# Performance work log

Hardware: AMD Instinct MI355X
Metric: run time of the kernel (lower is better)

The kernel has to match this reference:

```python
import jax, jax.numpy as jnp
import numpy as np

N0, N1, N2 = 20000, 15000, 15000
N = N0 + N1 + N2            # total nodes
E = 800000                  # edges (avg degree 16)
H, C = 128, 64


def setup_inputs() -> dict:
    key = jax.random.key(0)
    ks = jax.random.split(key, 16)
    s = 0.05  # weight scale
    return {
        "feat0": jax.random.normal(ks[0], (N0, 512), jnp.float32),
        "feat1": jax.random.normal(ks[1], (N1, 256), jnp.float32),
        "feat2": jax.random.normal(ks[2], (N2, 128), jnp.float32),
        "W0": jax.random.normal(ks[3], (512, H), jnp.float32) * s,
        "b0": jnp.zeros((H,), jnp.float32),
        "W1": jax.random.normal(ks[4], (256, H), jnp.float32) * s,
        "b1": jnp.zeros((H,), jnp.float32),
        "W2": jax.random.normal(ks[5], (128, H), jnp.float32) * s,
        "b2": jnp.zeros((H,), jnp.float32),
        "bias_l0": jnp.zeros((H,), jnp.float32),
        "W_l1": jax.random.normal(ks[6], (H, H), jnp.float32) * s,
        "b_l1": jnp.zeros((H,), jnp.float32),
        "W_l2": jax.random.normal(ks[7], (H, C), jnp.float32) * s,
        "b_l2": jnp.zeros((C,), jnp.float32),
        "src": jax.random.randint(ks[8], (E,), 0, N, jnp.int32),
        "dst": jax.random.randint(ks[9], (E,), 0, N, jnp.int32),
    }


def _norms(src, dst):
    # DGL GraphConv norm='both': src side uses out-degree, dst side in-degree
    ones = jnp.ones((E,), jnp.float32)
    deg_out = jax.ops.segment_sum(ones, src, num_segments=N)
    deg_in = jax.ops.segment_sum(ones, dst, num_segments=N)
    return jnp.maximum(deg_out, 1.0) ** -0.5, jnp.maximum(deg_in, 1.0) ** -0.5


def _agg(h, src, dst, norm_src, norm_dst):
    # normalized sparse aggregation: D_in^{-1/2} A D_out^{-1/2} h
    m = (h * norm_src[:, None])[src]                     # [E, d] gather
    a = jax.ops.segment_sum(m, dst, num_segments=N)      # [N, d] scatter-add
    return a * norm_dst[:, None]


def reference(feat0, feat1, feat2, W0, b0, W1, b1, W2, b2,
              bias_l0, W_l1, b_l1, W_l2, b_l2, src, dst):
    # per-node-type linear projections, concatenated along node axis
    h = jnp.concatenate([feat0 @ W0 + b0,
                         feat1 @ W1 + b1,
                         feat2 @ W2 + b2], axis=0)       # [N, H]
    ns, nd = _norms(src, dst)
    # layer 0: GraphConv(weight=False) -> agg + bias + relu (dropout = eval identity)
    h = jax.nn.relu(_agg(h, src, dst, ns, nd) + bias_l0)
    # layer 1: agg + linear + relu
    h = jax.nn.relu(_agg(h, src, dst, ns, nd) @ W_l1 + b_l1)
    # layer 2: agg + linear (no activation)
    h = _agg(h, src, dst, ns, nd) @ W_l2 + b_l2          # [N, C]
    return h
```

## Files before the change

kernel.cpp:

```cpp
#include <hip/hip_runtime.h>
#include <hip/hip_fp16.h>

#define N_NODES 50000
#define N0_ 20000
#define N1_ 15000
#define N2_ 15000
#define E_EDGES 800000
#define H_ 128
#define C_ 64

#define PB0 ((N0_ + 63) / 64)
#define PB1 ((N1_ + 63) / 64)
#define PB2 ((N2_ + 63) / 64)
#define PB_TOTAL (PB0 + PB1 + PB2)
#define EB ((E_EDGES + 255) / 256)
#define SB ((N_NODES + 255) / 256)

typedef _Float16 half4_t __attribute__((ext_vector_type(4)));
typedef _Float16 half8_t __attribute__((ext_vector_type(8)));
typedef float f32x4 __attribute__((ext_vector_type(4)));

__device__ __forceinline__ float4 load_a4(const float* A, size_t idx) {
    return *reinterpret_cast<const float4*>(&A[idx]);
}
__device__ __forceinline__ float4 load_a4(const __half* A, size_t idx) {
    __half2 p0 = *reinterpret_cast<const __half2*>(&A[idx]);
    __half2 p1 = *reinterpret_cast<const __half2*>(&A[idx + 2]);
    float2 f0 = __half22float2(p0), f1 = __half22float2(p1);
    return make_float4(f0.x, f0.y, f1.x, f1.y);
}


template <int TN, bool BIAS, bool RELU, bool SCALE, typename IT, typename OT>
__device__ __forceinline__ void gemm_block(
    const IT* __restrict__ A, const float* __restrict__ W,
    const float* __restrict__ bias, const float* __restrict__ rowscale,
    OT* __restrict__ out, int M, int K, int m0, float* As, float* Bs) {
    constexpr int NJ = TN / 32;
    constexpr int TN4 = TN / 4;
    int tid = threadIdx.x;
    int tx = tid & 31;
    int ty = tid >> 5;

    float acc[8][NJ];
#pragma unroll
    for (int i = 0; i < 8; i++)
#pragma unroll
        for (int j = 0; j < NJ; j++) acc[i][j] = 0.f;

    for (int k0 = 0; k0 < K; k0 += 32) {
#pragma unroll
        for (int t0 = 0; t0 < 2; t0++) {
            int t = tid + t0 * 256;
            int row = t >> 3;
            int c = t & 7;
            float4 v = make_float4(0.f, 0.f, 0.f, 0.f);
            if (m0 + row < M) v = load_a4(A, (size_t)(m0 + row) * K + k0 + c * 4);
            As[(c * 4 + 0) * 68 + row] = v.x;
            As[(c * 4 + 1) * 68 + row] = v.y;
            As[(c * 4 + 2) * 68 + row] = v.z;
            As[(c * 4 + 3) * 68 + row] = v.w;
        }
#pragma unroll
        for (int t0 = 0; t0 < 32 * TN4 / 256; t0++) {
            int t = tid + t0 * 256;
            int r = t / TN4;
            int c4 = t % TN4;
            *reinterpret_cast<float4*>(&Bs[r * TN + c4 * 4]) =
                *reinterpret_cast<const float4*>(&W[(size_t)(k0 + r) * TN + c4 * 4]);
        }
        __syncthreads();
#pragma unroll 8
        for (int k = 0; k < 32; k++) {
            float4 a0 = *reinterpret_cast<float4*>(&As[k * 68 + ty * 8]);
            float4 a1 = *reinterpret_cast<float4*>(&As[k * 68 + ty * 8 + 4]);
            float ar[8] = {a0.x, a0.y, a0.z, a0.w, a1.x, a1.y, a1.z, a1.w};
            float br[NJ];
#pragma unroll
            for (int j = 0; j < NJ; j++) br[j] = Bs[k * TN + tx + 32 * j];
#pragma unroll
            for (int i = 0; i < 8; i++)
#pragma unroll
                for (int j = 0; j < NJ; j++) acc[i][j] = fmaf(ar[i], br[j], acc[i][j]);
        }
        __syncthreads();
    }
#pragma unroll
    for (int i = 0; i < 8; i++) {
        int row = m0 + ty * 8 + i;
        if (row < M) {
            float sc = SCALE ? rowscale[row] : 1.f;
#pragma unroll
            for (int j = 0; j < NJ; j++) {
                float v = acc[i][j] + (BIAS ? bias[tx + 32 * j] : 0.f);
                if (RELU) v = fmaxf(v, 0.f);
                v *= sc;
                out[(size_t)row * TN + tx + 32 * j] = (OT)v;
            }
        }
    }
}


__global__ __launch_bounds__(256) void k1_proj_rank(
    const float* __restrict__ feat0, const float* __restrict__ feat1, const float* __restrict__ feat2,
    const float* __restrict__ W0, const float* __restrict__ b0,
    const float* __restrict__ W1, const float* __restrict__ b1,
    const float* __restrict__ W2, const float* __restrict__ b2,
    __half* __restrict__ h0h,
    const int* __restrict__ src, const int* __restrict__ dst,
    int* __restrict__ cnt, int* __restrict__ degO, int* __restrict__ rank) {
    __shared__ _Float16 smem[15360];
    int bid = blockIdx.x;
    int tid = threadIdx.x;
    if (bid < PB_TOTAL) {
        const float* A; const float* Wp; const float* bp; int M, K, m0;
        if (bid < PB0) {
            A = feat0; Wp = W0; bp = b0; M = N0_; K = 512; m0 = bid * 64;
        } else if (bid < PB0 + PB1) {
            A = feat1; Wp = W1; bp = b1; M = N1_; K = 256; m0 = (bid - PB0) * 64;
        } else {
            A = feat2; Wp = W2; bp = b2; M = N2_; K = 128; m0 = (bid - PB0 - PB1) * 64;
        }
        size_t obase = (bid < PB0) ? 0 : ((bid < PB0 + PB1) ? (size_t)N0_ * H_
                                                            : (size_t)(N0_ + N1_) * H_);
        _Float16* Ah = smem;
        _Float16* Al = smem + 2560;
        _Float16* Bh = smem + 5120;
        _Float16* Bl = smem + 10240;

        int wv = tid >> 6;
        int lane = tid & 63;
        int lm = lane & 15;
        int ks = lane >> 4;

        f32x4 acc[8];
#pragma unroll
        for (int j = 0; j < 8; j++)
#pragma unroll
            for (int r = 0; r < 4; r++) acc[j][r] = 0.f;

        for (int k0 = 0; k0 < K; k0 += 32) {
#pragma unroll
            for (int t0 = 0; t0 < 2; t0++) {
                int idx = tid + t0 * 256;
                int row = idx >> 3;
                int c = idx & 7;
                float4 v = make_float4(0.f, 0.f, 0.f, 0.f);
                if (m0 + row < M)
                    v = *reinterpret_cast<const float4*>(&A[(size_t)(m0 + row) * K + k0 + c * 4]);
                _Float16 hx = (_Float16)v.x, hy = (_Float16)v.y;
                _Float16 hz = (_Float16)v.z, hw = (_Float16)v.w;
                half4_t hi = {hx, hy, hz, hw};
                half4_t lo = {(_Float16)(v.x - (float)hx), (_Float16)(v.y - (float)hy),
                              (_Float16)(v.z - (float)hz), (_Float16)(v.w - (float)hw)};
                *reinterpret_cast<half4_t*>(&Ah[row * 40 + c * 4]) = hi;
                *reinterpret_cast<half4_t*>(&Al[row * 40 + c * 4]) = lo;
            }
#pragma unroll
            for (int t0 = 0; t0 < 4; t0++) {
                int idx = tid + t0 * 256;
                int kr = idx >> 5;
                int c4 = idx & 31;
                float4 v = *reinterpret_cast<const float4*>(&Wp[(size_t)(k0 + kr) * 128 + c4 * 4]);
                float f[4] = {v.x, v.y, v.z, v.w};
#pragma unroll
                for (int j = 0; j < 4; j++) {
                    _Float16 hi = (_Float16)f[j];
                    Bh[(c4 * 4 + j) * 40 + kr] = hi;
                    Bl[(c4 * 4 + j) * 40 + kr] = (_Float16)(f[j] - (float)hi);
                }
            }
            __syncthreads();
            half8_t ah = *reinterpret_cast<half8_t*>(&Ah[(16 * wv + lm) * 40 + ks * 8]);
            half8_t al = *reinterpret_cast<half8_t*>(&Al[(16 * wv + lm) * 40 + ks * 8]);
#pragma unroll
            for (int j = 0; j < 8; j++) {
                half8_t bh = *reinterpret_cast<half8_t*>(&Bh[(16 * j + lm) * 40 + ks * 8]);
                half8_t bl = *reinterpret_cast<half8_t*>(&Bl[(16 * j + lm) * 40 + ks * 8]);
                acc[j] = __builtin_amdgcn_mfma_f32_16x16x32_f16(ah, bh, acc[j], 0, 0, 0);
                acc[j] = __builtin_amdgcn_mfma_f32_16x16x32_f16(al, bh, acc[j], 0, 0, 0);
                acc[j] = __builtin_amdgcn_mfma_f32_16x16x32_f16(ah, bl, acc[j], 0, 0, 0);
            }
            __syncthreads();
        }
#pragma unroll
        for (int j = 0; j < 8; j++) {
            int colg = 16 * j + lm;
            float bb = bp[colg];
#pragma unroll
            for (int r = 0; r < 4; r++) {
                int row = m0 + 16 * wv + ks * 4 + r;
                if (row < M) h0h[obase + (size_t)row * H_ + colg] = (__half)(acc[j][r] + bb);
            }
        }
    } else {
        int e = (bid - PB_TOTAL) * 256 + tid;
        if (e < E_EDGES) {
            rank[e] = atomicAdd(&cnt[dst[e]], 1);
            atomicAdd(&degO[src[e]], 1);
        }
    }
}


__global__ __launch_bounds__(256) void scan1_kernel(
    const int* __restrict__ cnt, int* __restrict__ pre, int* __restrict__ blocksum) {
    __shared__ int buf[256];
    int t = threadIdx.x;
    int i = blockIdx.x * 256 + t;
    int tot = (i < N_NODES) ? cnt[i] : 0;
    buf[t] = tot;
    __syncthreads();
#pragma unroll
    for (int off = 1; off < 256; off <<= 1) {
        int v = (t >= off) ? buf[t - off] : 0;
        __syncthreads();
        buf[t] += v;
        __syncthreads();
    }
    if (i < N_NODES) pre[i] = buf[t] - tot;
    if (t == 255) blocksum[blockIdx.x] = buf[255];
}

__global__ __launch_bounds__(256) void scan2_kernel(
    const int* __restrict__ blocksum, int* __restrict__ blockoff, int* __restrict__ rowptr) {
    __shared__ int buf[256];
    int t = threadIdx.x;
    int v = (t < SB) ? blocksum[t] : 0;
    buf[t] = v;
    __syncthreads();
#pragma unroll
    for (int off = 1; off < 256; off <<= 1) {
        int u = (t >= off) ? buf[t - off] : 0;
        __syncthreads();
        buf[t] += u;
        __syncthreads();
    }
    if (t < SB) blockoff[t] = buf[t] - v;
    if (t == 255) rowptr[N_NODES] = buf[255];
}

__global__ __launch_bounds__(256) void scan3_fill_kernel(
    const int* __restrict__ cnt, const int* __restrict__ degO, const int* __restrict__ pre,
    const int* __restrict__ blockoff, int* __restrict__ rowptr,
    float* __restrict__ ns, float* __restrict__ nd,
    const int* __restrict__ src, const int* __restrict__ dst,
    const int* __restrict__ rank, int* __restrict__ col) {
    int bid = blockIdx.x;
    if (bid < SB) {
        int i = bid * 256 + threadIdx.x;
        if (i < N_NODES) {
            rowptr[i] = blockoff[bid] + pre[i];
            ns[i] = rsqrtf(fmaxf((float)degO[i], 1.0f));
            nd[i] = rsqrtf(fmaxf((float)cnt[i], 1.0f));
        }
    } else {
        int e = (bid - SB) * 256 + threadIdx.x;
        if (e < E_EDGES) {
            int d = dst[e];
            int rp = blockoff[d >> 8] + pre[d];
            col[rp + rank[e]] = src[e];
        }
    }
}


template <int CH, int NSLOAD, int EPI, int OUTH>
__global__ __launch_bounds__(256) void agg_h_kernel(
    const __half* __restrict__ h, const int* __restrict__ rowptr,
    const int* __restrict__ col, const float* __restrict__ ns,
    const float* __restrict__ nd, const float* __restrict__ bias,
    void* __restrict__ out) {
    constexpr int L = CH / 8;
    constexpr int EPW = 64 / L;
    int node = blockIdx.x * 4 + (threadIdx.x >> 6);
    if (node >= N_NODES) return;
    int lane = threadIdx.x & 63;
    int li = lane & (L - 1);
    int g = lane / L;
    const uint4* __restrict__ h8 = (const uint4*)h;
    int beg = rowptr[node], end = rowptr[node + 1];
    float a0[8] = {0.f, 0.f, 0.f, 0.f, 0.f, 0.f, 0.f, 0.f};
    float a1[8] = {0.f, 0.f, 0.f, 0.f, 0.f, 0.f, 0.f, 0.f};
    union U8 { uint4 u; __half2 h2[4]; };
    int e = beg + g;
    for (; e + EPW < end; e += 2 * EPW) {
        int s0 = col[e], s1 = col[e + EPW];
        U8 u0, u1;
        u0.u = h8[(size_t)s0 * L + li];
        u1.u = h8[(size_t)s1 * L + li];
        float w0 = NSLOAD ? ns[s0] : 1.f;
        float w1 = NSLOAD ? ns[s1] : 1.f;
#pragma unroll
        for (int p = 0; p < 4; p++) {
            float2 f0 = __half22float2(u0.h2[p]);
            float2 f1 = __half22float2(u1.h2[p]);
            if (NSLOAD) {
                a0[2 * p] = fmaf(w0, f0.x, a0[2 * p]);
                a0[2 * p + 1] = fmaf(w0, f0.y, a0[2 * p + 1]);
                a1[2 * p] = fmaf(w1, f1.x, a1[2 * p]);
                a1[2 * p + 1] = fmaf(w1, f1.y, a1[2 * p + 1]);
            } else {
                a0[2 * p] += f0.x;
                a0[2 * p + 1] += f0.y;
                a1[2 * p] += f1.x;
                a1[2 * p + 1] += f1.y;
            }
        }
    }
    if (e < end) {
        int s = col[e];
        U8 u0;
        u0.u = h8[(size_t)s * L + li];
        float w0 = NSLOAD ? ns[s] : 1.f;
#pragma unroll
        for (int p = 0; p < 4; p++) {
            float2 f0 = __half22float2(u0.h2[p]);
            if (NSLOAD) {
                a0[2 * p] = fmaf(w0, f0.x, a0[2 * p]);
                a0[2 * p + 1] = fmaf(w0, f0.y, a0[2 * p + 1]);
            } else {
                a0[2 * p] += f0.x;
                a0[2 * p + 1] += f0.y;
            }
        }
    }
#pragma unroll
    for (int j = 0; j < 8; j++) {
        float v = a0[j] + a1[j];
#pragma unroll
        for (int off = 32; off >= L; off >>= 1) v += __shfl_xor(v, off);
        a0[j] = v;
    }
    if (lane < L) {
        float w = nd[node];
#pragma unroll
        for (int j = 0; j < 8; j++) a0[j] *= w;
        if (EPI == 1) {
            float sc = ns[node];
#pragma unroll
            for (int j = 0; j < 8; j++)
                a0[j] = fmaxf(a0[j] + bias[li * 8 + j], 0.f) * sc;
        } else if (EPI == 2) {
#pragma unroll
            for (int j = 0; j < 8; j++) a0[j] += bias[li * 8 + j];
        }
        if (OUTH) {
            union { uint4 u; __half hh[8]; } cv;
#pragma unroll
            for (int j = 0; j < 8; j++) cv.hh[j] = __float2half(a0[j]);
            ((uint4*)out)[(size_t)node * L + li] = cv.u;
        } else {
            float4* o4 = (float4*)out;
            o4[(size_t)node * (CH / 4) + li * 2] = make_float4(a0[0], a0[1], a0[2], a0[3]);
            o4[(size_t)node * (CH / 4) + li * 2 + 1] = make_float4(a0[4], a0[5], a0[6], a0[7]);
        }
    }
}


template <int TN, bool BIAS, bool RELU, bool SCALE, typename IT, typename OT>
__global__ __launch_bounds__(256) void gemm_kernel(
    const IT* __restrict__ A, const float* __restrict__ W,
    const float* __restrict__ bias, const float* __restrict__ rowscale,
    OT* __restrict__ out, int M, int K) {
    __shared__ float As[32 * 68];
    __shared__ float Bs[32 * TN];
    gemm_block<TN, BIAS, RELU, SCALE, IT, OT>(A, W, bias, rowscale, out, M, K, blockIdx.x * 64, As, Bs);
}


extern "C" void kernel_launch(void* const* d_in, const int* in_sizes, int n_in,
                              void* d_out, int out_size, void* d_ws, size_t ws_size,
                              hipStream_t stream) {
    const float* feat0 = (const float*)d_in[0];
    const float* feat1 = (const float*)d_in[1];
    const float* feat2 = (const float*)d_in[2];
    const float* W0 = (const float*)d_in[3];
    const float* b0 = (const float*)d_in[4];
    const float* W1 = (const float*)d_in[5];
    const float* b1 = (const float*)d_in[6];
    const float* W2 = (const float*)d_in[7];
    const float* b2 = (const float*)d_in[8];
    const float* bias_l0 = (const float*)d_in[9];
    const float* W_l1 = (const float*)d_in[10];
    const float* b_l1 = (const float*)d_in[11];
    const float* W_l2 = (const float*)d_in[12];
    const float* b_l2 = (const float*)d_in[13];
    const int* src = (const int*)d_in[14];
    const int* dst = (const int*)d_in[15];
    float* out = (float*)d_out;

    char* ws = (char*)d_ws;
    size_t off = 0;
    auto alloc = [&](size_t bytes) {
        size_t cur = off;
        off += (bytes + 255) & ~(size_t)255;
        return cur;
    };
    size_t h0h_off = alloc((size_t)N_NODES * H_ * 2);
    size_t h1h_off = alloc((size_t)N_NODES * H_ * 2);
    size_t hAh_off = alloc((size_t)N_NODES * H_ * 2);
    size_t hBh_off = alloc((size_t)N_NODES * H_ * 2);
    size_t h2h_off = alloc((size_t)N_NODES * C_ * 2);
    size_t cnt_off = alloc((size_t)N_NODES * 4);
    size_t degO_off = alloc((size_t)N_NODES * 4);
    size_t ns_off = alloc((size_t)N_NODES * 4);
    size_t nd_off = alloc((size_t)N_NODES * 4);
    size_t rowptr_off = alloc((size_t)(N_NODES + 1) * 4);
    size_t rank_off = alloc((size_t)E_EDGES * 4);
    size_t col_off = alloc((size_t)E_EDGES * 4);
    size_t pre_off = alloc((size_t)N_NODES * 4);
    size_t bsum_off = alloc((size_t)SB * 4);
    size_t boff_off = alloc((size_t)SB * 4);

    __half* h0h = (__half*)(ws + h0h_off);
    __half* h1h = (__half*)(ws + h1h_off);
    __half* hAh = (__half*)(ws + hAh_off);
    __half* hBh = (__half*)(ws + hBh_off);
    __half* h2h = (__half*)(ws + h2h_off);
    int* cnt = (int*)(ws + cnt_off);
    int* degO = (int*)(ws + degO_off);
    float* ns = (float*)(ws + ns_off);
    float* nd = (float*)(ws + nd_off);
    int* rowptr = (int*)(ws + rowptr_off);
    int* rank = (int*)(ws + rank_off);
    int* col = (int*)(ws + col_off);
    int* pre = (int*)(ws + pre_off);
    int* bsum = (int*)(ws + bsum_off);
    int* boff = (int*)(ws + boff_off);

    hipMemsetAsync(ws + cnt_off, 0, ns_off - cnt_off, stream);

    k1_proj_rank<<<PB_TOTAL + EB, 256, 0, stream>>>(
        feat0, feat1, feat2, W0, b0, W1, b1, W2, b2, h0h, src, dst, cnt, degO, rank);
    scan1_kernel<<<SB, 256, 0, stream>>>(cnt, pre, bsum);
    scan2_kernel<<<1, 256, 0, stream>>>(bsum, boff, rowptr);
    scan3_fill_kernel<<<SB + EB, 256, 0, stream>>>(
        cnt, degO, pre, boff, rowptr, ns, nd, src, dst, rank, col);

    const int AGB = (N_NODES + 3) / 4;
    agg_h_kernel<128, 1, 1, 1><<<AGB, 256, 0, stream>>>(h0h, rowptr, col, ns, nd, bias_l0, h1h);
    agg_h_kernel<128, 0, 0, 1><<<AGB, 256, 0, stream>>>(h1h, rowptr, col, ns, nd, nullptr, hAh);
    gemm_kernel<128, true, true, true, __half, __half><<<(N_NODES + 63) / 64, 256, 0, stream>>>(
        hAh, W_l1, b_l1, ns, hBh, N_NODES, 128);
    gemm_kernel<64, false, false, false, __half, __half><<<(N_NODES + 63) / 64, 256, 0, stream>>>(
        hBh, W_l2, nullptr, nullptr, h2h, N_NODES, 128);
    agg_h_kernel<64, 0, 2, 0><<<AGB, 256, 0, stream>>>(h2h, rowptr, col, ns, nd, b_l2, out);
}
```

Before: 308.1 us.

## Replace split-fp16 MFMA projection with packed fp16 dot2 SIMT GEMM

Drops the hi/lo split fp16 MFMA projection (three MFMAs per tile) and uses plain fp16 inputs with v_dot2 fp32-accumulate on the vector ALUs. A small prepass kernel packs W0/W1/W2 into fp16 pairs along K, so the main kernel copies B tiles straight into shared memory without converting them. This lowers precision, because inputs are now a single fp16 rather than compensated, and moves the work from matrix cores to SIMT dot products. It also adds one extra kernel launch.

```diff
diff --git a/kernel.cpp b/kernel.cpp
--- a/kernel.cpp
+++ b/kernel.cpp
@@ -16,9 +16,20 @@
 #define EB ((E_EDGES + 255) / 256)
 #define SB ((N_NODES + 255) / 256)
 
-typedef _Float16 half4_t __attribute__((ext_vector_type(4)));
-typedef _Float16 half8_t __attribute__((ext_vector_type(8)));
-typedef float f32x4 __attribute__((ext_vector_type(4)));
+#define WT2_0 0
+#define WT2_1 32768
+#define WT2_2 49152
+#define WT2_TOTAL 57344
+
+typedef _Float16 h2_t __attribute__((ext_vector_type(2)));
+
+__device__ __forceinline__ float fdot2f(h2_t a, h2_t b, float c) {
+#if __has_builtin(__builtin_amdgcn_fdot2)
+    return __builtin_amdgcn_fdot2(a, b, c, false);
+#else
+    return fmaf((float)a[0], (float)b[0], fmaf((float)a[1], (float)b[1], c));
+#endif
+}
 
 __device__ __forceinline__ float4 load_a4(const float* A, size_t idx) {
     return *reinterpret_cast<const float4*>(&A[idx]);
@@ -102,43 +113,54 @@
 }
 
 
+__global__ __launch_bounds__(256) void wt2p_kernel(
+    const float* __restrict__ W0, const float* __restrict__ W1, const float* __restrict__ W2,
+    h2_t* __restrict__ Wt2) {
+    int t = blockIdx.x * 256 + threadIdx.x;
+    if (t >= WT2_TOTAL) return;
+    const float* W;
+    int rel;
+    if (t < WT2_1) { W = W0; rel = t; }
+    else if (t < WT2_2) { W = W1; rel = t - WT2_1; }
+    else { W = W2; rel = t - WT2_2; }
+    int k2 = rel >> 7;
+    int n = rel & 127;
+    h2_t p = {(_Float16)W[(size_t)(2 * k2) * 128 + n], (_Float16)W[(size_t)(2 * k2 + 1) * 128 + n]};
+    Wt2[t] = p;
+}
+
+
 __global__ __launch_bounds__(256) void k1_proj_rank(
     const float* __restrict__ feat0, const float* __restrict__ feat1, const float* __restrict__ feat2,
-    const float* __restrict__ W0, const float* __restrict__ b0,
-    const float* __restrict__ W1, const float* __restrict__ b1,
-    const float* __restrict__ W2, const float* __restrict__ b2,
+    const h2_t* __restrict__ Wt2,
+    const float* __restrict__ b0, const float* __restrict__ b1, const float* __restrict__ b2,
     __half* __restrict__ h0h,
     const int* __restrict__ src, const int* __restrict__ dst,
     int* __restrict__ cnt, int* __restrict__ degO, int* __restrict__ rank) {
-    __shared__ _Float16 smem[15360];
+    __shared__ h2_t As2[16 * 68];
+    __shared__ h2_t Bs2[16 * 128];
     int bid = blockIdx.x;
     int tid = threadIdx.x;
     if (bid < PB_TOTAL) {
-        const float* A; const float* Wp; const float* bp; int M, K, m0;
+        const float* A; const float* bp; const h2_t* Wp; int M, K, m0;
+        size_t obase;
         if (bid < PB0) {
-            A = feat0; Wp = W0; bp = b0; M = N0_; K = 512; m0 = bid * 64;
+            A = feat0; bp = b0; Wp = Wt2 + WT2_0; M = N0_; K = 512; m0 = bid * 64; obase = 0;
         } else if (bid < PB0 + PB1) {
-            A = feat1; Wp = W1; bp = b1; M = N1_; K = 256; m0 = (bid - PB0) * 64;
+            A = feat1; bp = b1; Wp = Wt2 + WT2_1; M = N1_; K = 256; m0 = (bid - PB0) * 64;
+            obase = (size_t)N0_ * H_;
         } else {
-            A = feat2; Wp = W2; bp = b2; M = N2_; K = 128; m0 = (bid - PB0 - PB1) * 64;
-        }
-        size_t obase = (bid < PB0) ? 0 : ((bid < PB0 + PB1) ? (size_t)N0_ * H_
-                                                            : (size_t)(N0_ + N1_) * H_);
-        _Float16* Ah = smem;
-        _Float16* Al = smem + 2560;
-        _Float16* Bh = smem + 5120;
-        _Float16* Bl = smem + 10240;
-
-        int wv = tid >> 6;
-        int lane = tid & 63;
-        int lm = lane & 15;
-        int ks = lane >> 4;
-
-        f32x4 acc[8];
-#pragma unroll
-        for (int j = 0; j < 8; j++)
-#pragma unroll
-            for (int r = 0; r < 4; r++) acc[j][r] = 0.f;
+            A = feat2; bp = b2; Wp = Wt2 + WT2_2; M = N2_; K = 128; m0 = (bid - PB0 - PB1) * 64;
+            obase = (size_t)(N0_ + N1_) * H_;
+        }
+        int tx = tid & 31;
+        int ty = tid >> 5;
+
+        float acc[8][4];
+#pragma unroll
+        for (int i = 0; i < 8; i++)
+#pragma unroll
+            for (int j = 0; j < 4; j++) acc[i][j] = 0.f;
 
         for (int k0 = 0; k0 < K; k0 += 32) {
 #pragma unroll
@@ -149,49 +171,54 @@
                 float4 v = make_float4(0.f, 0.f, 0.f, 0.f);
                 if (m0 + row < M)
                     v = *reinterpret_cast<const float4*>(&A[(size_t)(m0 + row) * K + k0 + c * 4]);
-                _Float16 hx = (_Float16)v.x, hy = (_Float16)v.y;
-                _Float16 hz = (_Float16)v.z, hw = (_Float16)v.w;
-                half4_t hi = {hx, hy, hz, hw};
-                half4_t lo = {(_Float16)(v.x - (float)hx), (_Float16)(v.y - (float)hy),
-                              (_Float16)(v.z - (float)hz), (_Float16)(v.w - (float)hw)};
-                *reinterpret_cast<half4_t*>(&Ah[row * 40 + c * 4]) = hi;
-                *reinterpret_cast<half4_t*>(&Al[row * 40 + c * 4]) = lo;
-            }
-#pragma unroll
-            for (int t0 = 0; t0 < 4; t0++) {
-                int idx = tid + t0 * 256;
-                int kr = idx >> 5;
-                int c4 = idx & 31;
-                float4 v = *reinterpret_cast<const float4*>(&Wp[(size_t)(k0 + kr) * 128 + c4 * 4]);
-                float f[4] = {v.x, v.y, v.z, v.w};
+                h2_t p0 = {(_Float16)v.x, (_Float16)v.y};
+                h2_t p1 = {(_Float16)v.z, (_Float16)v.w};
+                As2[(c * 2) * 68 + row] = p0;
+                As2[(c * 2 + 1) * 68 + row] = p1;
+            }
+            {
+                const uint4* g = reinterpret_cast<const uint4*>(Wp + (size_t)(k0 / 2) * 128);
+                uint4* l = reinterpret_cast<uint4*>(Bs2);
+                l[tid] = g[tid];
+                l[tid + 256] = g[tid + 256];
+            }
+            __syncthreads();
+#pragma unroll
+            for (int k2 = 0; k2 < 16; k2++) {
+                float4 fa0 = *reinterpret_cast<float4*>(&As2[k2 * 68 + ty * 8]);
+                float4 fa1 = *reinterpret_cast<float4*>(&As2[k2 * 68 + ty * 8 + 4]);
+                h2_t a0 = __builtin_bit_cast(h2_t, fa0.x);
+                h2_t a1 = __builtin_bit_cast(h2_t, fa0.y);
+                h2_t a2 = __builtin_bit_cast(h2_t, fa0.z);
+                h2_t a3 = __builtin_bit_cast(h2_t, fa0.w);
+                h2_t a4 = __builtin_bit_cast(h2_t, fa1.x);
+                h2_t a5 = __builtin_bit_cast(h2_t, fa1.y);
+                h2_t a6 = __builtin_bit_cast(h2_t, fa1.z);
+                h2_t a7 = __builtin_bit_cast(h2_t, fa1.w);
 #pragma unroll
                 for (int j = 0; j < 4; j++) {
-                    _Float16 hi = (_Float16)f[j];
-                    Bh[(c4 * 4 + j) * 40 + kr] = hi;
-                    Bl[(c4 * 4 + j) * 40 + kr] = (_Float16)(f[j] - (float)hi);
+                    h2_t b = Bs2[k2 * 128 + tx + 32 * j];
+                    acc[0][j] = fdot2f(a0, b, acc[0][j]);
+                    acc[1][j] = fdot2f(a1, b, acc[1][j]);
+                    acc[2][j] = fdot2f(a2, b, acc[2][j]);
+                    acc[3][j] = fdot2f(a3, b, acc[3][j]);
+                    acc[4][j] = fdot2f(a4, b, acc[4][j]);
+                    acc[5][j] = fdot2f(a5, b, acc[5][j]);
+                    acc[6][j] = fdot2f(a6, b, acc[6][j]);
+                    acc[7][j] = fdot2f(a7, b, acc[7][j]);
                 }
             }
             __syncthreads();
-            half8_t ah = *reinterpret_cast<half8_t*>(&Ah[(16 * wv + lm) * 40 + ks * 8]);
-            half8_t al = *reinterpret_cast<half8_t*>(&Al[(16 * wv + lm) * 40 + ks * 8]);
-#pragma unroll
-            for (int j = 0; j < 8; j++) {
-                half8_t bh = *reinterpret_cast<half8_t*>(&Bh[(16 * j + lm) * 40 + ks * 8]);
-                half8_t bl = *reinterpret_cast<half8_t*>(&Bl[(16 * j + lm) * 40 + ks * 8]);
-                acc[j] = __builtin_amdgcn_mfma_f32_16x16x32_f16(ah, bh, acc[j], 0, 0, 0);
-                acc[j] = __builtin_amdgcn_mfma_f32_16x16x32_f16(al, bh, acc[j], 0, 0, 0);
-                acc[j] = __builtin_amdgcn_mfma_f32_16x16x32_f16(ah, bl, acc[j], 0, 0, 0);
-            }
-            __syncthreads();
-        }
-#pragma unroll
-        for (int j = 0; j < 8; j++) {
-            int colg = 16 * j + lm;
-            float bb = bp[colg];
-#pragma unroll
-            for (int r = 0; r < 4; r++) {
-                int row = m0 + 16 * wv + ks * 4 + r;
-                if (row < M) h0h[obase + (size_t)row * H_ + colg] = (__half)(acc[j][r] + bb);
+        }
+#pragma unroll
+        for (int i = 0; i < 8; i++) {
+            int row = m0 + ty * 8 + i;
+            if (row < M) {
+#pragma unroll
+                for (int j = 0; j < 4; j++) {
+                    float v = acc[i][j] + bp[tx + 32 * j];
+                    h0h[obase + (size_t)row * H_ + tx + 32 * j] = (__half)v;
+                }
             }
         }
     } else {
@@ -399,6 +426,7 @@
         off += (bytes + 255) & ~(size_t)255;
         return cur;
     };
+    size_t Wt2_off = alloc((size_t)WT2_TOTAL * 4);
     size_t h0h_off = alloc((size_t)N_NODES * H_ * 2);
     size_t h1h_off = alloc((size_t)N_NODES * H_ * 2);
     size_t hAh_off = alloc((size_t)N_NODES * H_ * 2);
@@ -415,6 +443,7 @@
     size_t bsum_off = alloc((size_t)SB * 4);
     size_t boff_off = alloc((size_t)SB * 4);
 
+    h2_t* Wt2 = (h2_t*)(ws + Wt2_off);
     __half* h0h = (__half*)(ws + h0h_off);
     __half* h1h = (__half*)(ws + h1h_off);
     __half* hAh = (__half*)(ws + hAh_off);
@@ -433,8 +462,9 @@
 
     hipMemsetAsync(ws + cnt_off, 0, ns_off - cnt_off, stream);
 
+    wt2p_kernel<<<(WT2_TOTAL + 255) / 256, 256, 0, stream>>>(W0, W1, W2, Wt2);
     k1_proj_rank<<<PB_TOTAL + EB, 256, 0, stream>>>(
-        feat0, feat1, feat2, W0, b0, W1, b1, W2, b2, h0h, src, dst, cnt, degO, rank);
+        feat0, feat1, feat2, Wt2, b0, b1, b2, h0h, src, dst, cnt, degO, rank);
     scan1_kernel<<<SB, 256, 0, stream>>>(cnt, pre, bsum);
     scan2_kernel<<<1, 256, 0, stream>>>(bsum, boff, rowptr);
     scan3_fill_kernel<<<SB + EB, 256, 0, stream>>>(
```

After: 285.9 us. 7.2% less time.
